# Performance work log

Measured on AMD Instinct MI355X. Metric: run time of the kernel, lower is better.

Reference implementation:

```python
import jax, jax.numpy as jnp
import numpy as np

D_MODEL = 256
N_HEADS = 8
D_HEAD = D_MODEL // N_HEADS
EMB = [16, 16, 16, 16]
CUMSUM = [0, 16, 32, 48, 64]
PSUM = sum(EMB)
LEVELS = [(122, 122), (61, 61), (31, 31), (16, 16)]
S_TOTAL = sum(h * w for h, w in LEVELS)
IMG = 976.0


def swap_pairs(x):
    # swap consecutive pairs along the leading (view) dim
    return x.reshape(-1, 2, *x.shape[1:])[:, ::-1].reshape(x.shape)


def grid_sample_bilinear(img, grid):
    # img: [B, H, W, D]; grid: [B, Q, 2] in [-1, 1]; align_corners=False, zero padding
    B, H, W, D = img.shape
    gx = (grid[..., 0] + 1.0) * (W * 0.5) - 0.5
    gy = (grid[..., 1] + 1.0) * (H * 0.5) - 0.5
    x0 = jnp.floor(gx)
    y0 = jnp.floor(gy)
    wx = (gx - x0)[..., None]
    wy = (gy - y0)[..., None]
    x0i = x0.astype(jnp.int32)
    y0i = y0.astype(jnp.int32)
    flat = img.reshape(B, H * W, D)

    def gather(xi, yi):
        valid = ((xi >= 0) & (xi < W) & (yi >= 0) & (yi < H)).astype(img.dtype)
        idx = jnp.clip(yi, 0, H - 1) * W + jnp.clip(xi, 0, W - 1)
        v = jnp.take_along_axis(flat, idx[..., None], axis=1)
        return v * valid[..., None]

    v00 = gather(x0i, y0i)
    v01 = gather(x0i + 1, y0i)
    v10 = gather(x0i, y0i + 1)
    v11 = gather(x0i + 1, y0i + 1)
    return (v00 * (1 - wx) * (1 - wy) + v01 * wx * (1 - wy)
            + v10 * (1 - wx) * wy + v11 * wx * wy)


def ms_deform_attn_core(value, shapes, sampling_locations, attention_weights):
    # value: [N, S, M, D]; sampling_locations: [N, Lq, M, P, 2]; attention_weights: [N, Lq, M, P]
    N, S, M, D = value.shape
    Lq = sampling_locations.shape[1]
    grids = 2.0 * sampling_locations - 1.0
    outs = []
    start = 0
    for lid, (H, W) in enumerate(shapes):
        p0, p1 = CUMSUM[lid], CUMSUM[lid + 1]
        Pl = p1 - p0
        v = value[:, start:start + H * W].reshape(N, H, W, M, D)
        v = v.transpose(0, 3, 1, 2, 4).reshape(N * M, H, W, D)
        g = grids[:, :, :, p0:p1].transpose(0, 2, 1, 3, 4).reshape(N * M, Lq * Pl, 2)
        outs.append(grid_sample_bilinear(v, g).reshape(N * M, Lq, Pl, D))
        start += H * W
    samp = jnp.concatenate(outs, axis=2)  # [N*M, Lq, Psum, D]
    w = attention_weights.transpose(0, 2, 1, 3).reshape(N * M, Lq, PSUM, 1)
    out = (samp * w).sum(axis=2)  # [N*M, Lq, D]
    return out.reshape(N, M, Lq, D).transpose(0, 2, 1, 3).reshape(N, Lq, M * D)


def _forward(query, input_flatten, reference_points, p_pfws, pt_transforms,
             W_val, b_val, W_attn, b_attn, W_out, b_out, shapes):
    N, Lq, _ = query.shape
    value = (input_flatten @ W_val.T + b_val).reshape(N, -1, N_HEADS, D_HEAD)
    attn = jax.nn.softmax((query @ W_attn.T + b_attn).reshape(N, Lq, N_HEADS, PSUM), axis=-1)

    # reverse 2x3 affine transform on reference points, scale to pixels
    A = pt_transforms[:, :, :2]
    t = pt_transforms[:, :, 2]
    orig = jnp.einsum('nij,nqj->nqi', jnp.linalg.inv(A), reference_points - t[:, None, :]) * IMG

    # epipolar line in the second (swapped) view: point(x) = ts + ms * x, x in [0, IMG]
    P1 = p_pfws
    P2 = swap_pairs(p_pfws)
    A1 = P1[:, :, :3]
    b1 = P1[:, :, 3]
    cam = -jnp.linalg.solve(A1, b1[:, :, None])[:, :, 0]  # camera center [N,3]
    uh = jnp.concatenate([orig, jnp.ones_like(orig[..., :1])], -1)
    ray = jnp.einsum('nij,nqj->nqi', jnp.linalg.inv(A1), uh - b1[:, None, :])  # [N,Q,3]

    def proj2(X):
        Xh = jnp.concatenate([X, jnp.ones_like(X[..., :1])], -1)
        y = jnp.einsum('nij,nqj->nqi', P2, Xh)
        return y[..., :2] / (y[..., 2:3] + 1e-8)

    ts = proj2(jnp.broadcast_to(cam[:, None, :], ray.shape))
    ms = (proj2(ray) - ts) / IMG

    locs = []
    for n_pts in EMB:
        xs = jnp.linspace(0.0, IMG, n_pts)
        locs.append(ts[:, :, None, :] + ms[:, :, None, :] * xs[None, None, :, None])
    loc = jnp.concatenate(locs, axis=2) / IMG  # [N, Lq, Psum, 2]

    T2 = swap_pairs(pt_transforms)
    loc = jnp.einsum('nij,nqpj->nqpi', T2[:, :, :2], loc) + T2[:, :, 2][:, None, None, :]
    loc = jnp.clip(loc, 0.0, 1.0)
    samp_loc = jnp.broadcast_to(loc[:, :, None, :, :], (N, Lq, N_HEADS, PSUM, 2))

    out = ms_deform_attn_core(swap_pairs(value), shapes, samp_loc, attn)
    return out @ W_out.T + b_out


def setup_inputs() -> dict:
    key = jax.random.key(0)
    ks = jax.random.split(key, 12)
    N, Lq = 4, 1000
    query = jax.random.normal(ks[0], (N, Lq, D_MODEL), jnp.float32)
    input_flatten = jax.random.normal(ks[1], (N, S_TOTAL, D_MODEL), jnp.float32)
    reference_points = jax.random.uniform(ks[2], (N, Lq, 2), jnp.float32)
    p_pfws = jnp.asarray(np.eye(3, 4), jnp.float32) + 0.05 * jax.random.normal(ks[3], (N, 3, 4), jnp.float32)
    pt_transforms = jnp.asarray(np.eye(2, 3), jnp.float32) + 0.05 * jax.random.normal(ks[4], (N, 2, 3), jnp.float32)
    W_val = 0.05 * jax.random.normal(ks[5], (D_MODEL, D_MODEL), jnp.float32)
    b_val = jnp.zeros((D_MODEL,), jnp.float32)
    W_attn = 0.05 * jax.random.normal(ks[6], (N_HEADS * PSUM, D_MODEL), jnp.float32)
    b_attn = jnp.zeros((N_HEADS * PSUM,), jnp.float32)
    W_out = 0.05 * jax.random.normal(ks[7], (D_MODEL, D_MODEL), jnp.float32)
    b_out = jnp.zeros((D_MODEL,), jnp.float32)
    input_spatial_shapes = np.asarray(LEVELS, np.int64)
    input_level_start_index = np.asarray(np.cumsum([0] + [h * w for h, w in LEVELS])[:-1], np.int64)
    return {"query": query, "input_flatten": input_flatten, "reference_points": reference_points,
            "p_pfws": p_pfws, "pt_transforms": pt_transforms,
            "W_val": W_val, "b_val": b_val, "W_attn": W_attn, "b_attn": b_attn,
            "W_out": W_out, "b_out": b_out,
            "input_spatial_shapes": input_spatial_shapes,
            "input_level_start_index": input_level_start_index}


def reference(query, input_flatten, reference_points, p_pfws, pt_transforms,
              W_val, b_val, W_attn, b_attn, W_out, b_out,
              input_spatial_shapes, input_level_start_index):
    shapes = [(int(h), int(w)) for h, w in np.asarray(input_spatial_shapes)]
    return _forward(query, input_flatten, reference_points, p_pfws, pt_transforms,
                    W_val, b_val, W_attn, b_attn, W_out, b_out, shapes)
```

## Files before the change

kernel.cpp:

```cpp
#include <hip/hip_runtime.h>
#include <hip/hip_bf16.h>
#include <math.h>

#define NB 4
#define LQ 1000
#define NHEAD 8
#define DHEAD 32
#define DMODEL 256
#define PSUM 64
#define STOT 19822
#define IMGF 976.0f
#define GK 256

__device__ __constant__ int c_LH[4] = {122, 61, 31, 16};
__device__ __constant__ int c_LW[4] = {122, 61, 31, 16};
__device__ __constant__ int c_LST[4] = {0, 14884, 18605, 19566};

typedef __attribute__((ext_vector_type(8))) short bf16x8;
typedef __attribute__((ext_vector_type(4))) float f32x4;

__device__ inline unsigned int pk2(float a, float b) {
    unsigned short ua = __bfloat16_as_ushort(__float2bfloat16(a));
    unsigned short ub = __bfloat16_as_ushort(__float2bfloat16(b));
    return (unsigned int)ua | ((unsigned int)ub << 16);
}
__device__ inline float bf2f(unsigned short u) {
    return __uint_as_float(((unsigned int)u) << 16);
}
__device__ inline bf16x8 cvt8(float4 u, float4 v) {
    union { unsigned int w[4]; bf16x8 h; } r;
    r.w[0] = pk2(u.x, u.y); r.w[1] = pk2(u.z, u.w);
    r.w[2] = pk2(v.x, v.y); r.w[3] = pk2(v.z, v.w);
    return r.h;
}
__device__ inline void gll16(const void* g, void* l) {
    __builtin_amdgcn_global_load_lds(
        (const __attribute__((address_space(1))) void*)g,
        (__attribute__((address_space(3))) void*)l, 16, 0, 0);
}
__device__ inline void hard_barrier() {
    asm volatile("" ::: "memory");
    __builtin_amdgcn_sched_barrier(0);
    __builtin_amdgcn_s_barrier();
    __builtin_amdgcn_sched_barrier(0);
    asm volatile("" ::: "memory");
}

__device__ inline void make_consts(int n, const float* p_pfws, const float* pt,
                                   float* consts) {
    const float* P1 = p_pfws + n * 12;
    const float* P2 = p_pfws + (n ^ 1) * 12;
    const float* T  = pt + n * 6;
    const float* T2 = pt + (n ^ 1) * 6;
    float* C = consts + n * 48;
    float det = T[0]*T[4] - T[1]*T[3];
    float idet = 1.0f/det;
    C[0] =  T[4]*idet; C[1] = -T[1]*idet;
    C[2] = -T[3]*idet; C[3] =  T[0]*idet;
    C[4] = T[2]; C[5] = T[5];
    float a=P1[0], b=P1[1], c=P1[2];
    float d=P1[4], e=P1[5], f=P1[6];
    float g=P1[8], h=P1[9], i=P1[10];
    float b10=P1[3], b11=P1[7], b12=P1[11];
    float A_=e*i-f*h, B_=c*h-b*i, Cc=b*f-c*e;
    float D_=f*g-d*i, E_=a*i-c*g, F_=c*d-a*f;
    float G_=d*h-e*g, H_=b*g-a*h, I_=a*e-b*d;
    float det3 = a*A_ + b*D_ + c*G_;
    float id3 = 1.0f/det3;
    C[6]=A_*id3;  C[7]=B_*id3;  C[8]=Cc*id3;
    C[9]=D_*id3;  C[10]=E_*id3; C[11]=F_*id3;
    C[12]=G_*id3; C[13]=H_*id3; C[14]=I_*id3;
    C[15]=b10; C[16]=b11; C[17]=b12;
    for (int k = 0; k < 12; ++k) C[18+k] = P2[k];
    float cam0 = -(C[6]*b10  + C[7]*b11  + C[8]*b12);
    float cam1 = -(C[9]*b10  + C[10]*b11 + C[11]*b12);
    float cam2 = -(C[12]*b10 + C[13]*b11 + C[14]*b12);
    float y0 = P2[0]*cam0 + P2[1]*cam1 + P2[2]*cam2  + P2[3];
    float y1 = P2[4]*cam0 + P2[5]*cam1 + P2[6]*cam2  + P2[7];
    float y2 = P2[8]*cam0 + P2[9]*cam1 + P2[10]*cam2 + P2[11];
    float inv = 1.0f/(y2 + 1e-8f);
    C[30] = y0*inv; C[31] = y1*inv;
    for (int k = 0; k < 6; ++k) C[32+k] = T2[k];
}

__global__ void prep(const float* __restrict__ Wv, const float* __restrict__ Wa,
                     const float* __restrict__ Wo,
                     unsigned short* __restrict__ wbv, unsigned short* __restrict__ wba,
                     unsigned short* __restrict__ wbo,
                     const float* __restrict__ p_pfws, const float* __restrict__ pt,
                     float* __restrict__ consts) {
    int bid = blockIdx.x;
    if (bid == 256) {
        int n = threadIdx.x;
        if (n < NB) make_consts(n, p_pfws, pt, consts);
        return;
    }
    int i = bid * 256 + threadIdx.x;
    const float* src; unsigned short* dst; int off;
    if (i < 16384)      { src = Wv; dst = wbv; off = i; }
    else if (i < 49152) { src = Wa; dst = wba; off = i - 16384; }
    else                { src = Wo; dst = wbo; off = i - 49152; }
    float4 f = ((const float4*)src)[off];
    ushort4 o;
    o.x = __bfloat16_as_ushort(__float2bfloat16(f.x));
    o.y = __bfloat16_as_ushort(__float2bfloat16(f.y));
    o.z = __bfloat16_as_ushort(__float2bfloat16(f.z));
    o.w = __bfloat16_as_ushort(__float2bfloat16(f.w));
    ((ushort4*)dst)[off] = o;
}

__global__ __launch_bounds__(256, 2)
void gemm_val_regB(const float* __restrict__ X, const unsigned short* __restrict__ Wb,
                   const float* __restrict__ bias, unsigned short* __restrict__ out,
                   int M, int T, int CHUNK) {
    __shared__ __align__(16) char As[2][32768];
    const int tid  = threadIdx.x;
    const int lane = tid & 63;
    const int wq   = tid >> 6;
    const int l15  = lane & 15;
    const int koct = lane >> 4;
    const int t0   = blockIdx.x * CHUNK;
    int nt = T - t0; if (nt > CHUNK) nt = CHUNK;
    if (nt <= 0) return;

    bf16x8 breg[8][4];
    #pragma unroll
    for (int ks = 0; ks < 8; ++ks)
        #pragma unroll
        for (int ni = 0; ni < 4; ++ni) {
            int col = wq * 64 + ni * 16 + l15;
            breg[ks][ni] = *(const bf16x8*)((const char*)Wb + (size_t)col * 512
                                            + ks * 64 + koct * 16);
        }
    float bias_v[4];
    #pragma unroll
    for (int ni = 0; ni < 4; ++ni) bias_v[ni] = bias[wq * 64 + ni * 16 + l15];

#define STAGE(g, b) do {                                                      \
        _Pragma("unroll") for (int j = 0; j < 8; ++j) {                       \
            int r_ = wq * 8 + j;                                              \
            int gr_ = (g) * 32 + r_; if (gr_ >= M) gr_ = M - 1;               \
            int lch_ = lane ^ (r_ & 7);                                       \
            gll16(X + (size_t)gr_ * GK + lch_ * 4, As[b] + r_ * 1024);        \
        } } while (0)

    STAGE(t0, 0);
    if (nt > 1) { STAGE(t0 + 1, 1); asm volatile("s_waitcnt vmcnt(8)" ::: "memory"); }
    else        {                   asm volatile("s_waitcnt vmcnt(0)" ::: "memory"); }
    hard_barrier();

#define COMPUTE_STORE(g, b) do {                                              \
        f32x4 acc[2][4] = {};                                                 \
        _Pragma("unroll") for (int ks = 0; ks < 8; ++ks) {                    \
            _Pragma("unroll") for (int mi = 0; mi < 2; ++mi) {                \
                int r_ = mi * 16 + l15;                                       \
                int ch_ = ks * 8 + koct * 2;                                  \
                float4 x0_ = *(const float4*)(As[b] + r_ * 1024 +             \
                                              ((ch_    ) ^ (r_ & 7)) * 16);   \
                float4 x1_ = *(const float4*)(As[b] + r_ * 1024 +             \
                                              ((ch_ + 1) ^ (r_ & 7)) * 16);   \
                bf16x8 af_ = cvt8(x0_, x1_);                                  \
                _Pragma("unroll") for (int ni = 0; ni < 4; ++ni)              \
                    acc[mi][ni] = __builtin_amdgcn_mfma_f32_16x16x32_bf16(    \
                        af_, breg[ks][ni], acc[mi][ni], 0, 0, 0);             \
            }                                                                 \
        }                                                                     \
        _Pragma("unroll") for (int mi = 0; mi < 2; ++mi) {                    \
            int rb_ = (g) * 32 + mi * 16 + (lane >> 4) * 4;                   \
            _Pragma("unroll") for (int j_ = 0; j_ < 4; ++j_) {                \
                int gr_ = rb_ + j_;                                           \
                if (gr_ < M) {                                                \
                    _Pragma("unroll") for (int ni = 0; ni < 4; ++ni)          \
                        out[(size_t)gr_ * DMODEL + wq * 64 + ni * 16 + l15] = \
                            __bfloat16_as_ushort(__float2bfloat16(            \
                                acc[mi][ni][j_] + bias_v[ni]));               \
                }                                                             \
            }                                                                 \
        } } while (0)

    for (int t = 0; t < nt; ++t) {
        COMPUTE_STORE(t0 + t, t & 1);
        if (t + 1 == nt) break;
        hard_barrier();
        if (t + 2 < nt) {
            STAGE(t0 + t + 2, t & 1);
            asm volatile("s_waitcnt vmcnt(8)" ::: "memory");
        } else {
            asm volatile("s_waitcnt vmcnt(0)" ::: "memory");
        }
        hard_barrier();
    }
#undef COMPUTE_STORE
#undef STAGE
}

template<bool OUT_BF16>
__global__ __launch_bounds__(256, 4)
void gemm64(const float* __restrict__ A, const unsigned short* __restrict__ Bb,
            const float* __restrict__ bias, void* __restrict__ outp,
            int M, int N) {
    __shared__ char smem[40960];
    char* asmem = smem;
    char* bsmem = smem + 8192;
    const int tid  = threadIdx.x;
    const int lane = tid & 63;
    const int w    = tid >> 6;
    const int l15  = lane & 15;
    const int koct = lane >> 4;
    const int i0 = blockIdx.x * 64;
    const int o0 = blockIdx.y * 256;

    const int s_row = tid >> 2;
    const int s_q   = tid & 3;
    int gr = i0 + s_row; gr = gr < M ? gr : M - 1;
    const float* aptr = A + (size_t)gr * GK + s_q * 16;
    const int s_sw = (s_row & 7) << 4;
    char* a_w0 = asmem + s_row * 128 + ((s_q * 32)      ^ s_sw);
    char* a_w1 = asmem + s_row * 128 + ((s_q * 32 + 16) ^ s_sw);

    const int b_sub = lane >> 3;
    const int b_kc  = (lane & 7) ^ b_sub;

    f32x4 acc[4][4] = {};
    float bias_v[4];
    #pragma unroll
    for (int ni = 0; ni < 4; ++ni) bias_v[ni] = bias[o0 + w * 64 + ni * 16 + l15];

    for (int t = 0; t < 4; ++t) {
        const int k0 = t * 64;
        #pragma unroll
        for (int j = 0; j < 8; ++j) {
            int cI = w * 8 + j;
            int col = cI * 8 + b_sub;
            gll16(Bb + (size_t)(o0 + col) * GK + k0 + b_kc * 8,
                  bsmem + cI * 1024);
        }
        {
            const float4* s = (const float4*)(aptr + k0);
            float4 f0 = s[0], f1 = s[1], f2 = s[2], f3 = s[3];
            uint4 wv0, wv1;
            wv0.x = pk2(f0.x,f0.y); wv0.y = pk2(f0.z,f0.w);
            wv0.z = pk2(f1.x,f1.y); wv0.w = pk2(f1.z,f1.w);
            wv1.x = pk2(f2.x,f2.y); wv1.y = pk2(f2.z,f2.w);
            wv1.z = pk2(f3.x,f3.y); wv1.w = pk2(f3.z,f3.w);
            *(uint4*)a_w0 = wv0;
            *(uint4*)a_w1 = wv1;
        }
        __syncthreads();
        #pragma unroll
        for (int ks = 0; ks < 2; ++ks) {
            const int kc = ks * 4 + koct;
            bf16x8 af[4], bfr[4];
            #pragma unroll
            for (int mi = 0; mi < 4; ++mi) {
                int r = mi * 16 + l15;
                af[mi] = *(const bf16x8*)(asmem + r * 128 + ((kc * 16) ^ ((r & 7) << 4)));
            }
            #pragma unroll
            for (int ni = 0; ni < 4; ++ni) {
                int c = w * 64 + ni * 16 + l15;
                bfr[ni] = *(const bf16x8*)(bsmem + c * 128 + ((kc * 16) ^ ((c & 7) << 4)));
            }
            #pragma unroll
            for (int mi = 0; mi < 4; ++mi)
                #pragma unroll
                for (int ni = 0; ni < 4; ++ni)
                    acc[mi][ni] = __builtin_amdgcn_mfma_f32_16x16x32_bf16(
                        af[mi], bfr[ni], acc[mi][ni], 0, 0, 0);
        }
        __syncthreads();
    }

    #pragma unroll
    for (int mi = 0; mi < 4; ++mi) {
        int rbase = i0 + mi * 16 + (lane >> 4) * 4;
        #pragma unroll
        for (int j = 0; j < 4; ++j) {
            int grow = rbase + j;
            if (grow < M) {
                #pragma unroll
                for (int ni = 0; ni < 4; ++ni) {
                    int gcol = o0 + w * 64 + ni * 16 + l15;
                    float v = acc[mi][ni][j] + bias_v[ni];
                    if (OUT_BF16)
                        ((unsigned short*)outp)[(size_t)grow * N + gcol] =
                            __bfloat16_as_ushort(__float2bfloat16(v));
                    else
                        ((float*)outp)[(size_t)grow * N + gcol] = v;
                }
            }
        }
    }
}

__global__ __launch_bounds__(256)
void fused_sample(const float* __restrict__ logits,
                  const float* __restrict__ ref_pts,
                  const unsigned short* __restrict__ value,
                  const float* __restrict__ consts,
                  float* __restrict__ attn_out) {
    int b = blockIdx.x;
    int n = b / LQ;
    int q = b - n * LQ;
    int tid = threadIdx.x;

    __shared__ float s_attn[512];
    __shared__ float s_loc[16][2];
    __shared__ int   s_idx[64][4];
    __shared__ float s_w[64][4];
    __shared__ float4 s_part[4][64];

    s_attn[tid]       = logits[(size_t)b * 512 + tid];
    s_attn[tid + 256] = logits[(size_t)b * 512 + tid + 256];
    __syncthreads();

    {
        int wave = tid >> 6, lane = tid & 63;
        for (int h = wave; h < NHEAD; h += 4) {
            float v = s_attn[h * 64 + lane];
            float mx = v;
            #pragma unroll
            for (int off = 32; off; off >>= 1) mx = fmaxf(mx, __shfl_xor(mx, off, 64));
            float e = expf(v - mx);
            float sm = e;
            #pragma unroll
            for (int off = 32; off; off >>= 1) sm += __shfl_xor(sm, off, 64);
            s_attn[h * 64 + lane] = e / sm;
        }
    }

    if (tid < 16) {
        const float* C = consts + n * 48;
        float rx = ref_pts[((size_t)n * LQ + q) * 2 + 0];
        float ry = ref_pts[((size_t)n * LQ + q) * 2 + 1];
        float dx = rx - C[4], dy = ry - C[5];
        float ox = (C[0]*dx + C[1]*dy) * IMGF;
        float oy = (C[2]*dx + C[3]*dy) * IMGF;
        float u0 = ox - C[15], u1 = oy - C[16], u2 = 1.0f - C[17];
        float r0 = C[6]*u0  + C[7]*u1  + C[8]*u2;
        float r1 = C[9]*u0  + C[10]*u1 + C[11]*u2;
        float r2 = C[12]*u0 + C[13]*u1 + C[14]*u2;
        float y0 = C[18]*r0 + C[19]*r1 + C[20]*r2 + C[21];
        float y1 = C[22]*r0 + C[23]*r1 + C[24]*r2 + C[25];
        float y2 = C[26]*r0 + C[27]*r1 + C[28]*r2 + C[29];
        float inv = 1.0f/(y2 + 1e-8f);
        float prx = y0*inv, pry = y1*inv;
        float ts0 = C[30], ts1 = C[31];
        float msx = (prx - ts0) / IMGF, msy = (pry - ts1) / IMGF;
        int j = tid;
        float xsj = IMGF * ((float)j / 15.0f);
        float lx = (ts0 + msx * xsj) / IMGF;
        float ly = (ts1 + msy * xsj) / IMGF;
        float Lx = C[32]*lx + C[33]*ly + C[34];
        float Ly = C[35]*lx + C[36]*ly + C[37];
        s_loc[j][0] = fminf(fmaxf(Lx, 0.0f), 1.0f);
        s_loc[j][1] = fminf(fmaxf(Ly, 0.0f), 1.0f);
    }
    __syncthreads();

    if (tid < 64) {
        int p = tid, lev = p >> 4, j = p & 15;
        int H = c_LH[lev], W = c_LW[lev], st = c_LST[lev];
        float gx = s_loc[j][0] * (float)W - 0.5f;
        float gy = s_loc[j][1] * (float)H - 0.5f;
        float x0f = floorf(gx), y0f = floorf(gy);
        float wx = gx - x0f, wy = gy - y0f;
        int x0 = (int)x0f, y0 = (int)y0f;
        int x1 = x0 + 1, y1 = y0 + 1;
        bool vx0 = (x0 >= 0) & (x0 < W), vx1 = (x1 >= 0) & (x1 < W);
        bool vy0 = (y0 >= 0) & (y0 < H), vy1 = (y1 >= 0) & (y1 < H);
        s_idx[p][0] = (vx0 & vy0) ? st + y0 * W + x0 : -1;  s_w[p][0] = (1.f-wx)*(1.f-wy);
        s_idx[p][1] = (vx1 & vy0) ? st + y0 * W + x1 : -1;  s_w[p][1] = wx*(1.f-wy);
        s_idx[p][2] = (vx0 & vy1) ? st + y1 * W + x0 : -1;  s_w[p][2] = (1.f-wx)*wy;
        s_idx[p][3] = (vx1 & vy1) ? st + y1 * W + x1 : -1;  s_w[p][3] = wx*wy;
    }
    __syncthreads();

    int wv = tid >> 6, lane = tid & 63;
    const unsigned short* vbase = value + (size_t)(n ^ 1) * STOT * DMODEL + lane * 4;
    int m = lane >> 3;
    float a0 = 0.f, a1 = 0.f, a2 = 0.f, a3 = 0.f;
    #pragma unroll 4
    for (int j = 0; j < 16; ++j) {
        int p = wv * 16 + j;
        float wa = s_attn[m * 64 + p];
        float s0 = 0.f, s1 = 0.f, s2 = 0.f, s3 = 0.f;
        #pragma unroll
        for (int cc = 0; cc < 4; ++cc) {
            int idx = s_idx[p][cc];
            if (idx >= 0) {
                ushort4 vv = *(const ushort4*)(vbase + (size_t)idx * DMODEL);
                float wgt = s_w[p][cc];
                s0 += wgt * bf2f(vv.x);
                s1 += wgt * bf2f(vv.y);
                s2 += wgt * bf2f(vv.z);
                s3 += wgt * bf2f(vv.w);
            }
        }
        a0 += wa * s0; a1 += wa * s1; a2 += wa * s2; a3 += wa * s3;
    }
    s_part[wv][lane] = make_float4(a0, a1, a2, a3);
    __syncthreads();

    const float* sp = (const float*)s_part;
    float r = sp[tid] + sp[256 + tid] + sp[512 + tid] + sp[768 + tid];
    attn_out[(size_t)b * DMODEL + tid] = r;
}

extern "C" void kernel_launch(void* const* d_in, const int* in_sizes, int n_in,
                              void* d_out, int out_size, void* d_ws, size_t ws_size,
                              hipStream_t stream) {
    const float* query         = (const float*)d_in[0];
    const float* input_flatten = (const float*)d_in[1];
    const float* ref_pts       = (const float*)d_in[2];
    const float* p_pfws        = (const float*)d_in[3];
    const float* pt            = (const float*)d_in[4];
    const float* W_val         = (const float*)d_in[5];
    const float* b_val         = (const float*)d_in[6];
    const float* W_attn        = (const float*)d_in[7];
    const float* b_attn        = (const float*)d_in[8];
    const float* W_out         = (const float*)d_in[9];
    const float* b_out         = (const float*)d_in[10];
    float* out = (float*)d_out;

    const int M = NB * STOT;
    const size_t value_bytes  = (size_t)M * DMODEL * 2;
    const size_t logits_bytes = (size_t)NB * LQ * 512 * 4;
    const size_t attn_bytes   = (size_t)NB * LQ * DMODEL * 4;
    const size_t consts_bytes = NB * 48 * 4;
    const size_t wv_bytes     = (size_t)DMODEL * DMODEL * 2;
    const size_t wa_bytes     = (size_t)512 * DMODEL * 2;
    const size_t wo_bytes     = (size_t)DMODEL * DMODEL * 2;
    const size_t need = value_bytes + logits_bytes + attn_bytes + consts_bytes
                      + wv_bytes + wa_bytes + wo_bytes;
    if (ws_size < need) return;

    char* p = (char*)d_ws;
    unsigned short* value = (unsigned short*)p;  p += value_bytes;
    float* logits   = (float*)p;                 p += logits_bytes;
    float* attn_out = (float*)p;                 p += attn_bytes;
    float* consts   = (float*)p;                 p += consts_bytes;
    unsigned short* wb_val  = (unsigned short*)p; p += wv_bytes;
    unsigned short* wb_attn = (unsigned short*)p; p += wa_bytes;
    unsigned short* wb_out  = (unsigned short*)p; p += wo_bytes;

    prep<<<257, 256, 0, stream>>>(W_val, W_attn, W_out, wb_val, wb_attn, wb_out,
                                  p_pfws, pt, consts);

    {
        const int T = (M + 31) / 32;
        const int CHUNK = 5;
        const int blocks = (T + CHUNK - 1) / CHUNK;
        gemm_val_regB<<<blocks, 256, 0, stream>>>(input_flatten, wb_val, b_val,
                                                  value, M, T, CHUNK);
    }
    {
        dim3 g((NB * LQ + 63) / 64, 2);
        gemm64<false><<<g, 256, 0, stream>>>(query, wb_attn, b_attn, logits, NB * LQ, 512);
    }
    fused_sample<<<NB * LQ, 256, 0, stream>>>(logits, ref_pts, value, consts, attn_out);
    {
        dim3 g((NB * LQ + 63) / 64, 1);
        gemm64<false><<<g, 256, 0, stream>>>(attn_out, wb_out, b_out, out, NB * LQ, DMODEL);
    }
}
```

Before: 96.29 us.

## Gather bilinear corner pairs as 16-byte rows and deepen value GEMM prefetch

The sampling kernel now treats the two horizontally adjacent corners as one contiguous 2-pixel span. Each half-wave loads 8 bf16 values per row, with out-of-bounds corners handled by shifting the base and zeroing weights. This removes per-corner validity branches and halves the number of gather instructions, combining the halves with a cross-lane shuffle. Separately, the value GEMM drops to one block per CU and relaxes its vmcnt waits to keep more loads in flight. The risk is lower occupancy in the GEMM and extra shuffle work in the sampler.

```diff
diff --git a/kernel.cpp b/kernel.cpp
--- a/kernel.cpp
+++ b/kernel.cpp
@@ -109,7 +109,7 @@
     ((ushort4*)dst)[off] = o;
 }
 
-__global__ __launch_bounds__(256, 2)
+__global__ __launch_bounds__(256, 1)
 void gemm_val_regB(const float* __restrict__ X, const unsigned short* __restrict__ Wb,
                    const float* __restrict__ bias, unsigned short* __restrict__ out,
                    int M, int T, int CHUNK) {
@@ -184,9 +184,9 @@
         hard_barrier();
         if (t + 2 < nt) {
             STAGE(t0 + t + 2, t & 1);
-            asm volatile("s_waitcnt vmcnt(8)" ::: "memory");
+            asm volatile("s_waitcnt vmcnt(40)" ::: "memory");
         } else {
-            asm volatile("s_waitcnt vmcnt(0)" ::: "memory");
+            asm volatile("s_waitcnt vmcnt(32)" ::: "memory");
         }
         hard_barrier();
     }
@@ -306,9 +306,10 @@
 
     __shared__ float s_attn[512];
     __shared__ float s_loc[16][2];
-    __shared__ int   s_idx[64][4];
+    __shared__ int   s_b0[64];
+    __shared__ int   s_b1[64];
     __shared__ float s_w[64][4];
-    __shared__ float4 s_part[4][64];
+    __shared__ float s_part[4][32][9];
 
     s_attn[tid]       = logits[(size_t)b * 512 + tid];
     s_attn[tid + 256] = logits[(size_t)b * 512 + tid + 256];
@@ -368,42 +369,63 @@
         int x0 = (int)x0f, y0 = (int)y0f;
         int x1 = x0 + 1, y1 = y0 + 1;
         bool vx0 = (x0 >= 0) & (x0 < W), vx1 = (x1 >= 0) & (x1 < W);
-        bool vy0 = (y0 >= 0) & (y0 < H), vy1 = (y1 >= 0) & (y1 < H);
-        s_idx[p][0] = (vx0 & vy0) ? st + y0 * W + x0 : -1;  s_w[p][0] = (1.f-wx)*(1.f-wy);
-        s_idx[p][1] = (vx1 & vy0) ? st + y0 * W + x1 : -1;  s_w[p][1] = wx*(1.f-wy);
-        s_idx[p][2] = (vx0 & vy1) ? st + y1 * W + x0 : -1;  s_w[p][2] = (1.f-wx)*wy;
-        s_idx[p][3] = (vx1 & vy1) ? st + y1 * W + x1 : -1;  s_w[p][3] = wx*wy;
+        int xb; float wl, wr;
+        if (vx0 & vx1)      { xb = x0;     wl = 1.f - wx; wr = wx;       }
+        else if (vx1)       { xb = x1;     wl = wx;       wr = 0.f;      }
+        else if (vx0)       { xb = x0 - 1; wl = 0.f;      wr = 1.f - wx; }
+        else                { xb = 0;      wl = 0.f;      wr = 0.f;      }
+        bool vy0 = (y0 >= 0) & (y0 < H);
+        bool vy1 = (y1 >= 0) & (y1 < H);
+        int b0 = st + (vy0 ? y0 : 0) * W + xb;
+        int b1 = st + (vy1 ? y1 : 0) * W + xb;
+        b0 = b0 < STOT - 2 ? b0 : STOT - 2;
+        b1 = b1 < STOT - 2 ? b1 : STOT - 2;
+        float fy0 = vy0 ? (1.f - wy) : 0.f;
+        float fy1 = vy1 ? wy : 0.f;
+        s_b0[p] = b0; s_b1[p] = b1;
+        s_w[p][0] = wl * fy0; s_w[p][1] = wr * fy0;
+        s_w[p][2] = wl * fy1; s_w[p][3] = wr * fy1;
     }
     __syncthreads();
 
     int wv = tid >> 6, lane = tid & 63;
-    const unsigned short* vbase = value + (size_t)(n ^ 1) * STOT * DMODEL + lane * 4;
-    int m = lane >> 3;
-    float a0 = 0.f, a1 = 0.f, a2 = 0.f, a3 = 0.f;
+    int half = lane >> 5, l31 = lane & 31;
+    const unsigned short* valb = value + (size_t)(n ^ 1) * STOT * DMODEL + lane * 8;
+    int m = l31 >> 2;
+    float a0=0.f,a1=0.f,a2=0.f,a3=0.f,a4=0.f,a5=0.f,a6=0.f,a7=0.f;
     #pragma unroll 4
     for (int j = 0; j < 16; ++j) {
         int p = wv * 16 + j;
-        float wa = s_attn[m * 64 + p];
-        float s0 = 0.f, s1 = 0.f, s2 = 0.f, s3 = 0.f;
-        #pragma unroll
-        for (int cc = 0; cc < 4; ++cc) {
-            int idx = s_idx[p][cc];
-            if (idx >= 0) {
-                ushort4 vv = *(const ushort4*)(vbase + (size_t)idx * DMODEL);
-                float wgt = s_w[p][cc];
-                s0 += wgt * bf2f(vv.x);
-                s1 += wgt * bf2f(vv.y);
-                s2 += wgt * bf2f(vv.z);
-                s3 += wgt * bf2f(vv.w);
-            }
-        }
-        a0 += wa * s0; a1 += wa * s1; a2 += wa * s2; a3 += wa * s3;
-    }
-    s_part[wv][lane] = make_float4(a0, a1, a2, a3);
+        float wa  = s_attn[m * 64 + p];
+        float wx0 = s_w[p][half];
+        float wx1 = s_w[p][half + 2];
+        bf16x8 v0 = *(const bf16x8*)(valb + (size_t)s_b0[p] * DMODEL);
+        bf16x8 v1 = *(const bf16x8*)(valb + (size_t)s_b1[p] * DMODEL);
+        float t0 = wx0 * bf2f((unsigned short)v0[0]) + wx1 * bf2f((unsigned short)v1[0]);
+        float t1 = wx0 * bf2f((unsigned short)v0[1]) + wx1 * bf2f((unsigned short)v1[1]);
+        float t2 = wx0 * bf2f((unsigned short)v0[2]) + wx1 * bf2f((unsigned short)v1[2]);
+        float t3 = wx0 * bf2f((unsigned short)v0[3]) + wx1 * bf2f((unsigned short)v1[3]);
+        float t4 = wx0 * bf2f((unsigned short)v0[4]) + wx1 * bf2f((unsigned short)v1[4]);
+        float t5 = wx0 * bf2f((unsigned short)v0[5]) + wx1 * bf2f((unsigned short)v1[5]);
+        float t6 = wx0 * bf2f((unsigned short)v0[6]) + wx1 * bf2f((unsigned short)v1[6]);
+        float t7 = wx0 * bf2f((unsigned short)v0[7]) + wx1 * bf2f((unsigned short)v1[7]);
+        t0 += __shfl_xor(t0, 32, 64);  t1 += __shfl_xor(t1, 32, 64);
+        t2 += __shfl_xor(t2, 32, 64);  t3 += __shfl_xor(t3, 32, 64);
+        t4 += __shfl_xor(t4, 32, 64);  t5 += __shfl_xor(t5, 32, 64);
+        t6 += __shfl_xor(t6, 32, 64);  t7 += __shfl_xor(t7, 32, 64);
+        a0 += wa * t0; a1 += wa * t1; a2 += wa * t2; a3 += wa * t3;
+        a4 += wa * t4; a5 += wa * t5; a6 += wa * t6; a7 += wa * t7;
+    }
+    if (half == 0) {
+        s_part[wv][l31][0] = a0; s_part[wv][l31][1] = a1;
+        s_part[wv][l31][2] = a2; s_part[wv][l31][3] = a3;
+        s_part[wv][l31][4] = a4; s_part[wv][l31][5] = a5;
+        s_part[wv][l31][6] = a6; s_part[wv][l31][7] = a7;
+    }
     __syncthreads();
 
-    const float* sp = (const float*)s_part;
-    float r = sp[tid] + sp[256 + tid] + sp[512 + tid] + sp[768 + tid];
+    float r = s_part[0][tid >> 3][tid & 7] + s_part[1][tid >> 3][tid & 7]
+            + s_part[2][tid >> 3][tid & 7] + s_part[3][tid >> 3][tid & 7];
     attn_out[(size_t)b * DMODEL + tid] = r;
 }
 
```

Result: no change. 97.35 us (+1.1%).
